# Optimization experiments

Hardware: AMD Instinct MI355X
Metric: run time of the kernel (lower is better)

Reference implementation:

```python
import jax, jax.numpy as jnp
import numpy as np

B = 256
WIN = 20          # input image side; 20 -> 12 -> 4 so num_routes = 32*4*4 = 512
ROUTES = 512
NCAPS = 10
DOUT = 16
DIN = 8
REC = 256 * WIN * WIN  # 102400


def _conv(x, w):
    return jax.lax.conv_general_dilated(x, w, (1, 1), 'VALID',
                                        dimension_numbers=('NCHW', 'OIHW', 'NCHW'))


def setup_inputs() -> dict:
    key = jax.random.key(0)
    ks = jax.random.split(key, 12)
    n = lambda k, shape, sc: (jax.random.normal(k, shape, jnp.float32) * sc)
    return {
        'data':    jax.random.normal(ks[0], (B, 1, WIN, WIN), jnp.float32),
        'conv1_w': n(ks[1], (256, 1, 9, 9), 0.1),
        'conv1_b': jnp.zeros((256,), jnp.float32),
        'prim_w':  n(ks[2], (8 * 32, 256, 9, 9), 0.007),  # 8 capsule convs fused: [8*32,256,9,9]
        'prim_b':  jnp.zeros((8 * 32,), jnp.float32),
        'W_digit': n(ks[3], (ROUTES, NCAPS, DOUT, DIN), 0.05),
        'dec_w1':  n(ks[4], (512, NCAPS * DOUT), 0.05),
        'dec_b1':  jnp.zeros((512,), jnp.float32),
        'dec_w2':  n(ks[5], (1024, 512), 0.04),
        'dec_b2':  jnp.zeros((1024,), jnp.float32),
        'dec_w3':  n(ks[6], (REC, 1024), 0.03),
        'dec_b3':  jnp.zeros((REC,), jnp.float32),
    }


def reference(data, conv1_w, conv1_b, prim_w, prim_b, W_digit,
              dec_w1, dec_b1, dec_w2, dec_b2, dec_w3, dec_b3):
    Bn = data.shape[0]
    # ConvLayer: 9x9 VALID conv + relu -> [B,256,12,12]
    h = jax.nn.relu(_conv(data, conv1_w) + conv1_b[None, :, None, None])
    # PrimaryCaps: 8 parallel convs (fused as one 256-out conv) -> [B,8,32,4,4]
    u = _conv(h, prim_w) + prim_b[None, :, None, None]
    H, W = u.shape[2], u.shape[3]
    u = u.reshape(Bn, 8, 32, H, W)
    # torch's u.view(B, 32*H*W, -1): raw row-major reshape of (8,32,H,W) -> (32*H*W, 8)
    u = u.reshape(Bn, 32 * H * W, 8)
    # vector squash over last (8-dim) axis
    sn = jnp.sum(u * u, axis=-1, keepdims=True)
    x = sn * u / ((1.0 + sn) * jnp.sqrt(sn))          # [B,R,8]
    # DigitCaps: u_hat[b,r,c,o] = W[r,c,o,i] x[b,r,i]
    u_hat = jnp.einsum('rcoi,bri->brco', W_digit, x)  # [B,R,10,16]
    b_ij = jnp.zeros((ROUTES, NCAPS), u_hat.dtype)    # shared over batch, as in original
    v = None
    for it in range(3):
        c = jax.nn.softmax(b_ij, axis=0)              # softmax over routes
        s = jnp.einsum('rc,brco->bco', c, u_hat)      # [B,10,16]
        # NOTE: original squash sums over a trailing dim of size 1 -> elementwise squash
        sq = s * s
        v = sq * s / ((1.0 + sq) * jnp.sqrt(sq))      # [B,10,16]
        if it < 2:
            a = jnp.einsum('brco,bco->brc', u_hat, v)
            b_ij = b_ij + jnp.mean(a, axis=0)
    # Decoder
    classes = jnp.sqrt(jnp.sum(v * v, axis=2))        # [B,10]
    classes = jax.nn.softmax(classes, axis=0)         # legacy F.softmax on 3D -> dim 0
    idx = jnp.argmax(classes, axis=1)                 # [B]
    masked = jax.nn.one_hot(idx, NCAPS, dtype=v.dtype)
    flat = (v * masked[:, :, None]).reshape(Bn, -1)   # [B,160]
    h1 = jax.nn.relu(flat @ dec_w1.T + dec_b1)
    h2 = jax.nn.relu(h1 @ dec_w2.T + dec_b2)
    rec = jax.nn.sigmoid(h2 @ dec_w3.T + dec_b3)
    return rec.reshape(-1, 256, WIN, WIN)
```

## Files before the change

kernel.cpp:

```cpp
#include <hip/hip_runtime.h>
#include <cmath>


constexpr int BATCH = 256;

enum { AM_PLAIN = 0, AM_CONV1 = 1 };
enum { EPI_NONE = 0, EPI_RELU = 1, EPI_SIG = 2, EPI_RELU_SPLIT = 3, EPI_RELU_H2B = 4 };

typedef short bf16x8 __attribute__((ext_vector_type(8)));
typedef unsigned short us8 __attribute__((ext_vector_type(8)));
typedef float f32x4 __attribute__((ext_vector_type(4)));

__device__ __forceinline__ unsigned short f2b(float v) {
  unsigned int u = __float_as_uint(v);
  u += 0x7FFFu + ((u >> 16) & 1u);
  return (unsigned short)(u >> 16);
}
__device__ __forceinline__ void split_bf(float v, unsigned short& h, unsigned short& l) {
  h = f2b(v);
  l = f2b(v - __uint_as_float(((unsigned int)h) << 16));
}

__device__ __forceinline__ void gload16(unsigned short* lds, const unsigned short* g) {
  __builtin_amdgcn_global_load_lds(
      (const __attribute__((address_space(1))) unsigned int*)(g),
      (__attribute__((address_space(3))) unsigned int*)(lds), 16, 0, 0);
}

template <int BM, int BN, int TM, int TN, int AMODE, int EPI>
__global__ __launch_bounds__(256, 2) void gemm_k(
    const float* __restrict__ A, const float* __restrict__ Bm,
    const float* __restrict__ bias, float* __restrict__ C,
    int M, int N, int K, int k_len,
    unsigned short* __restrict__ Chi, unsigned short* __restrict__ Clo) {
  static_assert(TM == 8 && TN == 8, "microtile fixed at 8x8");
  constexpr int BK = 8;
  constexpr int TX = BN / TN;

  const int tid = threadIdx.x;
  const int tx = tid % TX;
  const int ty = tid / TX;
  const int n0 = blockIdx.x * BN;
  const int m0 = blockIdx.y * BM;
  const int k_begin = blockIdx.z * k_len;
  const int k_end = k_begin + k_len;
  C += (size_t)blockIdx.z * (size_t)M * (size_t)N;

  __shared__ float As[BK][BM + 4];
  __shared__ float Bs[BK][BN + 4];

  float acc[TM][TN] = {};

  for (int kt = k_begin; kt < k_end; kt += BK) {
    __syncthreads();
    for (int base = tid * 4; base < BM * BK; base += 1024) {
      int ml = base / BK;
      int kl = base % BK;
#pragma unroll
      for (int j = 0; j < 4; j++) {
        int k = kt + kl + j;
        float v = 0.f;
        if (k < k_end) {
          if constexpr (AMODE == AM_PLAIN) {
            v = A[(size_t)(m0 + ml) * K + k];
          } else {
            int m = m0 + ml;
            int b = m / 144, p = m - b * 144;
            int py = p / 12, px = p - py * 12;
            int ky = k / 9, kx = k - ky * 9;
            v = A[b * 400 + (py + ky) * 20 + (px + kx)];
          }
        }
        As[kl + j][ml] = v;
      }
    }
    for (int base = tid * 4; base < BN * BK; base += 1024) {
      int nl = base / BK;
      int kl = base % BK;
#pragma unroll
      for (int j = 0; j < 4; j++) {
        int k = kt + kl + j;
        float v = 0.f;
        if (k < k_end) v = Bm[(size_t)(n0 + nl) * K + k];
        Bs[kl + j][nl] = v;
      }
    }
    __syncthreads();
#pragma unroll
    for (int kk = 0; kk < BK; kk++) {
      float af[TM], bf[TN];
      const float4* ap = reinterpret_cast<const float4*>(&As[kk][ty * TM]);
      reinterpret_cast<float4*>(af)[0] = ap[0];
      reinterpret_cast<float4*>(af)[1] = ap[1];
      const float4* bp = reinterpret_cast<const float4*>(&Bs[kk][tx * TN]);
      reinterpret_cast<float4*>(bf)[0] = bp[0];
      reinterpret_cast<float4*>(bf)[1] = bp[1];
#pragma unroll
      for (int i = 0; i < TM; i++)
#pragma unroll
        for (int j = 0; j < TN; j++) acc[i][j] += af[i] * bf[j];
    }
  }

#pragma unroll
  for (int i = 0; i < TM; i++) {
    int m = m0 + ty * TM + i;
#pragma unroll
    for (int j = 0; j < TN; j++) {
      int n = n0 + tx * TN + j;
      float v = acc[i][j];
      if constexpr (EPI == EPI_RELU) {
        v += bias[n];
        v = fmaxf(v, 0.f);
        C[(size_t)m * N + n] = v;
      } else if constexpr (EPI == EPI_SIG) {
        v += bias[n];
        v = 1.f / (1.f + expf(-v));
        C[(size_t)m * N + n] = v;
      } else if constexpr (EPI == EPI_RELU_SPLIT) {
        v += bias[n];
        v = fmaxf(v, 0.f);
        unsigned short hs, ls;
        split_bf(v, hs, ls);
        Chi[(size_t)m * N + n] = hs;
        Clo[(size_t)m * N + n] = ls;
      } else if constexpr (EPI == EPI_RELU_H2B) {
        v += bias[n];
        v = fmaxf(v, 0.f);
        Chi[(size_t)m * N + n] = f2b(v);
      } else {
        C[(size_t)m * N + n] = v;
      }
    }
  }
}

__global__ void transpose_w_k(const float* __restrict__ w,
                              unsigned short* __restrict__ hi,
                              unsigned short* __restrict__ lo) {
  __shared__ unsigned short shi[10368], slo[10368];
  const int n = blockIdx.x >> 1;
  const int h = blockIdx.x & 1;
  const int tid = threadIdx.x;
  const float* src = w + n * 20736 + h * 10368;
  for (int i = tid; i < 10368; i += 256) {
    float v = src[i];
    int cin_l = i / 81, kk = i - cin_l * 81;
    int idx = kk * 128 + ((cin_l + 2 * kk) & 127);
    unsigned short hb, lb;
    split_bf(v, hb, lb);
    shi[idx] = hb;
    slo[idx] = lb;
  }
  __syncthreads();
  unsigned short* dh = hi + n * 20736 + h * 128;
  unsigned short* dl = lo + n * 20736 + h * 128;
  for (int j = tid; j < 10368; j += 256) {
    int kk = j >> 7, cin_l = j & 127;
    int idx = (j & ~127) + ((cin_l + 2 * kk) & 127);
    dh[kk * 256 + cin_l] = shi[idx];
    dl[kk * 256 + cin_l] = slo[idx];
  }
}

__global__ __launch_bounds__(256, 2) void prim_mfma_k(
    const unsigned short* __restrict__ Ahi, const unsigned short* __restrict__ Alo,
    const unsigned short* __restrict__ Bhi, const unsigned short* __restrict__ Blo,
    float* __restrict__ part) {
  __shared__ unsigned short Ah[128 * 64], Al[128 * 64];
  __shared__ unsigned short Bh[128 * 64], Bl[128 * 64];

  const int tid = threadIdx.x;
  const int wave = tid >> 6, lane = tid & 63;
  const int wm = (wave >> 1) * 64, wn = (wave & 1) * 64;
  const int cl = lane & 15, rq = lane >> 4;
  const int n0 = blockIdx.x * 128;
  const int m0 = blockIdx.y * 128;
  const int z = blockIdx.z;
  const int k_begin = z * 1728, k_end = k_begin + 1728;

  int s_ldso[4];
  int s_arow[4];
  int s_cp8[4];
  size_t s_gb[4];
#pragma unroll
  for (int t = 0; t < 4; t++) {
    int g = (wave * 4 + t) * 64 + lane;
    int row = g >> 3, c = g & 7;
    int cp = c ^ (row & 7);
    s_ldso[t] = (wave * 4 + t) * 512;
    s_cp8[t] = cp * 8;
    int m = m0 + row;
    int b = m >> 4, q = m & 15;
    int y = q >> 2, xx = q & 3;
    s_arow[t] = b * 144 + y * 12 + xx;
    s_gb[t] = (size_t)(n0 + row) * 20736 + cp * 8;
  }

  f32x4 acc[4][4];
#pragma unroll
  for (int i = 0; i < 4; i++)
#pragma unroll
    for (int j = 0; j < 4; j++) acc[i][j] = f32x4{0.f, 0.f, 0.f, 0.f};

  for (int kt = k_begin; kt < k_end; kt += 64) {
    const int kk = kt >> 8;
    const int cin0 = kt & 255;
    const int dy = kk / 9, dx = kk - dy * 9;
    const int dyx = dy * 12 + dx;
    __syncthreads();
#pragma unroll
    for (int t = 0; t < 4; t++) {
      size_t ga = ((size_t)(s_arow[t] + dyx) << 8) + cin0 + s_cp8[t];
      size_t gb = s_gb[t] + kt;
      gload16(&Ah[s_ldso[t]], Ahi + ga);
      gload16(&Al[s_ldso[t]], Alo + ga);
      gload16(&Bh[s_ldso[t]], Bhi + gb);
      gload16(&Bl[s_ldso[t]], Blo + gb);
    }
    __syncthreads();

#pragma unroll
    for (int ko = 0; ko < 64; ko += 32) {
      const int cb = ko >> 3;
      bf16x8 a_hi[4], b_hi[4], t[4];
#pragma unroll
      for (int im = 0; im < 4; im++) {
        int r = wm + im * 16 + cl;
        a_hi[im] = *(const bf16x8*)&Ah[r * 64 + (((cb + rq) ^ (cl & 7)) << 3)];
      }
#pragma unroll
      for (int in = 0; in < 4; in++) {
        int r = wn + in * 16 + cl;
        b_hi[in] = *(const bf16x8*)&Bh[r * 64 + (((cb + rq) ^ (cl & 7)) << 3)];
      }
#pragma unroll
      for (int im = 0; im < 4; im++)
#pragma unroll
        for (int in = 0; in < 4; in++)
          acc[im][in] = __builtin_amdgcn_mfma_f32_16x16x32_bf16(a_hi[im], b_hi[in],
                                                                acc[im][in], 0, 0, 0);
#pragma unroll
      for (int in = 0; in < 4; in++) {
        int r = wn + in * 16 + cl;
        t[in] = *(const bf16x8*)&Bl[r * 64 + (((cb + rq) ^ (cl & 7)) << 3)];
      }
#pragma unroll
      for (int im = 0; im < 4; im++)
#pragma unroll
        for (int in = 0; in < 4; in++)
          acc[im][in] = __builtin_amdgcn_mfma_f32_16x16x32_bf16(a_hi[im], t[in],
                                                                acc[im][in], 0, 0, 0);
#pragma unroll
      for (int im = 0; im < 4; im++) {
        int r = wm + im * 16 + cl;
        t[im] = *(const bf16x8*)&Al[r * 64 + (((cb + rq) ^ (cl & 7)) << 3)];
      }
#pragma unroll
      for (int im = 0; im < 4; im++)
#pragma unroll
        for (int in = 0; in < 4; in++)
          acc[im][in] = __builtin_amdgcn_mfma_f32_16x16x32_bf16(t[im], b_hi[in],
                                                                acc[im][in], 0, 0, 0);
    }
  }

  float* Cp = part + (size_t)z * 1048576;
#pragma unroll
  for (int in = 0; in < 4; in++) {
    int n = n0 + wn + in * 16 + cl;
#pragma unroll
    for (int im = 0; im < 4; im++)
#pragma unroll
      for (int r = 0; r < 4; r++) {
        int m = m0 + wm + im * 16 + rq * 4 + r;
        Cp[(size_t)m * 256 + n] = acc[im][in][r];
      }
  }
}

__global__ __launch_bounds__(256, 2) void dec3_mfma_k(
    const unsigned short* __restrict__ Ab,
    const float* __restrict__ Bw,
    const float* __restrict__ bias,
    float* __restrict__ C) {
  constexpr int K = 1024, N = 102400;
  __shared__ unsigned short As[256 * 64];
  __shared__ unsigned short Bs[64 * 64];

  const int tid = threadIdx.x;
  const int wave = tid >> 6, lane = tid & 63;
  const int cl = lane & 15, rq = lane >> 4;
  const int n0 = blockIdx.x * 64;

  f32x4 acc[4][4];
#pragma unroll
  for (int i = 0; i < 4; i++)
#pragma unroll
    for (int j = 0; j < 4; j++) acc[i][j] = f32x4{0.f, 0.f, 0.f, 0.f};

  for (int kt = 0; kt < K; kt += 64) {
    __syncthreads();
#pragma unroll
    for (int j = 0; j < 8; j++) {
      int g = j * 256 + tid;
      int row = g >> 3, c = g & 7;
      int ld = row * 64 + ((c ^ (row & 7)) << 3);
      *(us8*)&As[ld] = *(const us8*)(Ab + (size_t)row * K + kt + c * 8);
    }
#pragma unroll
    for (int j = 0; j < 2; j++) {
      int g = j * 256 + tid;
      int row = g >> 3, c = g & 7;
      int ld = row * 64 + ((c ^ (row & 7)) << 3);
      const float* src = Bw + (size_t)(n0 + row) * K + kt + c * 8;
      float4 v0 = *(const float4*)src;
      float4 v1 = *(const float4*)(src + 4);
      us8 h;
      h[0] = f2b(v0.x); h[1] = f2b(v0.y); h[2] = f2b(v0.z); h[3] = f2b(v0.w);
      h[4] = f2b(v1.x); h[5] = f2b(v1.y); h[6] = f2b(v1.z); h[7] = f2b(v1.w);
      *(us8*)&Bs[ld] = h;
    }
    __syncthreads();
#pragma unroll
    for (int ko = 0; ko < 64; ko += 32) {
      const int cb = ko >> 3;
      bf16x8 af[4], bq[4];
#pragma unroll
      for (int im = 0; im < 4; im++) {
        int r = wave * 64 + im * 16 + cl;
        af[im] = *(const bf16x8*)&As[r * 64 + (((cb + rq) ^ (cl & 7)) << 3)];
      }
#pragma unroll
      for (int in = 0; in < 4; in++) {
        int r = in * 16 + cl;
        bq[in] = *(const bf16x8*)&Bs[r * 64 + (((cb + rq) ^ (cl & 7)) << 3)];
      }
#pragma unroll
      for (int im = 0; im < 4; im++)
#pragma unroll
        for (int in = 0; in < 4; in++)
          acc[im][in] = __builtin_amdgcn_mfma_f32_16x16x32_bf16(af[im], bq[in],
                                                                acc[im][in], 0, 0, 0);
    }
  }

#pragma unroll
  for (int in = 0; in < 4; in++) {
    int n = n0 + in * 16 + cl;
    float bn = bias[n];
#pragma unroll
    for (int im = 0; im < 4; im++)
#pragma unroll
      for (int r = 0; r < 4; r++) {
        int m = wave * 64 + im * 16 + rq * 4 + r;
        float v = acc[im][in][r] + bn;
        v = 1.f / (1.f + expf(-v));
        C[(size_t)m * N + n] = v;
      }
  }
}

__global__ void red_squash_k(const float* __restrict__ part,
                             const float* __restrict__ prim_b,
                             float* __restrict__ x) {
  const int chg = blockIdx.x;
  const int b = blockIdx.y;
  const int tid = threadIdx.x;
  const int ch_l = tid & 15;
  const int q = tid >> 4;
  const int ch = chg * 16 + ch_l;

  float val = prim_b[ch];
#pragma unroll
  for (int z = 0; z < 12; z++) val += part[z * 1048576 + (b * 16 + q) * 256 + ch];

  __shared__ float su[16][17];
  su[q][ch_l] = val;
  __syncthreads();

  const int vec = tid >> 3;
  const int i = tid & 7;
  const int ch_l2 = vec >> 1;
  const int t = vec & 1;
  float sn = 0.f;
#pragma unroll
  for (int ii = 0; ii < 8; ii++) {
    float e = su[8 * t + ii][ch_l2];
    sn += e * e;
  }
  float factor = sn / ((1.f + sn) * sqrtf(sn));
  float e = su[8 * t + i][ch_l2];
  int chh = chg * 16 + ch_l2;
  int d8 = chh >> 5, d32 = chh & 31;
  int r = d8 * 64 + d32 * 2 + t;
  x[b * 4096 + r * 8 + i] = e * factor;
}

__global__ void uhat_k(const float* __restrict__ W, const float* __restrict__ x,
                       float* __restrict__ uhat) {
  const int r = blockIdx.x;
  const int tid = threadIdx.x;
  __shared__ float Wl[8 * 160];
  __shared__ float xl[256 * 8];
  for (int t = tid; t < 1280; t += 256) {
    int co = t >> 3, i = t & 7;
    Wl[i * 160 + co] = W[r * 1280 + t];
  }
  for (int t = tid; t < 2048; t += 256) {
    int b = t >> 3, i = t & 7;
    xl[t] = x[b * 4096 + r * 8 + i];
  }
  __syncthreads();
  for (int item = tid; item < 256 * 160; item += 256) {
    int b = item / 160;
    int co = item - b * 160;
    float acc = 0.f;
#pragma unroll
    for (int i = 0; i < 8; i++) acc += Wl[i * 160 + co] * xl[b * 8 + i];
    uhat[b * 81920 + r * 160 + co] = acc;
  }
}

__global__ void zero_b_k(float* __restrict__ bij) {
  int id = blockIdx.x * 256 + threadIdx.x;
  if (id < 5120) bij[id] = 0.f;
}

__global__ void route_iter_k(const float* __restrict__ uhat,
                             const float* __restrict__ c_rc,
                             float* __restrict__ v_out,
                             float* __restrict__ a_buf,
                             int use_uniform, int do_update) {
  const int b = blockIdx.x;
  const int tid = threadIdx.x;
  __shared__ float c_l[5120];
  __shared__ float v_l[160];
  if (!use_uniform) {
    for (int t = tid; t < 5120; t += 256) c_l[t] = c_rc[t];
  }
  __syncthreads();
  if (tid < 160) {
    const float* up = uhat + b * 81920 + tid;
    const int cls = tid >> 4;
    float acc = 0.f;
    if (use_uniform) {
#pragma unroll 8
      for (int r = 0; r < 512; r++) acc += up[r * 160];
      acc *= (1.f / 512.f);
    } else {
#pragma unroll 8
      for (int r = 0; r < 512; r++) acc += c_l[r * 10 + cls] * up[r * 160];
    }
    float sq = acc * acc;
    float vv = sq * acc / ((1.f + sq) * sqrtf(sq));
    v_l[tid] = vv;
    v_out[b * 160 + tid] = vv;
  }
  __syncthreads();
  if (do_update) {
    for (int item = tid; item < 5120; item += 256) {
      int r = item / 10;
      int c = item - r * 10;
      const float* up2 = uhat + b * 81920 + r * 160 + c * 16;
      float a = 0.f;
#pragma unroll
      for (int o = 0; o < 16; o++) a += up2[o] * v_l[c * 16 + o];
      a_buf[b * 5120 + item] = a;
    }
  }
}

__global__ void bupd_k(const float* __restrict__ a_buf, float* __restrict__ bij) {
  int id = blockIdx.x * 256 + threadIdx.x;
  if (id >= 5120) return;
  float s = 0.f;
  for (int b = 0; b < BATCH; b++) s += a_buf[b * 5120 + id];
  bij[id] += s * (1.f / 256.f);
}

__global__ void softmax_b_k(const float* __restrict__ bij, float* __restrict__ c_rc) {
  const int tid = threadIdx.x;
  __shared__ float Ml[10], Sl[10];
  if (tid < 10) {
    float m = -1e30f;
    for (int r = 0; r < 512; r++) m = fmaxf(m, bij[r * 10 + tid]);
    float s = 0.f;
    for (int r = 0; r < 512; r++) s += expf(bij[r * 10 + tid] - m);
    Ml[tid] = m;
    Sl[tid] = s;
  }
  __syncthreads();
  if (tid < 512) {
    for (int c = 0; c < 10; c++)
      c_rc[tid * 10 + c] = expf(bij[tid * 10 + c] - Ml[c]) / Sl[c];
  }
}

__global__ void classes_k(const float* __restrict__ v, float* __restrict__ sel,
                          int* __restrict__ idxb) {
  const int b = threadIdx.x;
  float cl[10], ex[10];
  for (int c = 0; c < 10; c++) {
    float s = 0.f;
    for (int o = 0; o < 16; o++) {
      float e = v[b * 160 + c * 16 + o];
      s += e * e;
    }
    cl[c] = sqrtf(s);
  }
  __shared__ float red[256];
  __shared__ float Mc[10], Sc[10];
  for (int c = 0; c < 10; c++) {
    red[b] = cl[c];
    __syncthreads();
    for (int s = 128; s > 0; s >>= 1) {
      if (b < s) red[b] = fmaxf(red[b], red[b + s]);
      __syncthreads();
    }
    if (b == 0) Mc[c] = red[0];
    __syncthreads();
  }
  for (int c = 0; c < 10; c++) {
    ex[c] = expf(cl[c] - Mc[c]);
    red[b] = ex[c];
    __syncthreads();
    for (int s = 128; s > 0; s >>= 1) {
      if (b < s) red[b] += red[b + s];
      __syncthreads();
    }
    if (b == 0) Sc[c] = red[0];
    __syncthreads();
  }
  float best = ex[0] / Sc[0];
  int bi = 0;
  for (int c = 1; c < 10; c++) {
    float p = ex[c] / Sc[c];
    if (p > best) { best = p; bi = c; }
  }
  idxb[b] = bi;
  for (int o = 0; o < 16; o++) sel[b * 16 + o] = v[b * 160 + bi * 16 + o];
}

__global__ void h1_k(const float* __restrict__ sel, const int* __restrict__ idxb,
                     const float* __restrict__ w1, const float* __restrict__ b1,
                     float* __restrict__ h1) {
  const int b = blockIdx.x;
  const int j = threadIdx.x;
  __shared__ float ssel[16];
  __shared__ int six;
  if (j < 16) ssel[j] = sel[b * 16 + j];
  if (j == 0) six = idxb[b];
  __syncthreads();
  const float* wrow = w1 + j * 160 + six * 16;
  float acc = b1[j];
#pragma unroll
  for (int o = 0; o < 16; o++) acc += ssel[o] * wrow[o];
  h1[b * 512 + j] = fmaxf(acc, 0.f);
}

extern "C" void kernel_launch(void* const* d_in, const int* in_sizes, int n_in,
                              void* d_out, int out_size, void* d_ws, size_t ws_size,
                              hipStream_t stream) {
  const float* data    = (const float*)d_in[0];
  const float* conv1_w = (const float*)d_in[1];
  const float* conv1_b = (const float*)d_in[2];
  const float* prim_w  = (const float*)d_in[3];
  const float* prim_b  = (const float*)d_in[4];
  const float* W_digit = (const float*)d_in[5];
  const float* dec_w1  = (const float*)d_in[6];
  const float* dec_b1  = (const float*)d_in[7];
  const float* dec_w2  = (const float*)d_in[8];
  const float* dec_b2  = (const float*)d_in[9];
  const float* dec_w3  = (const float*)d_in[10];
  const float* dec_b3  = (const float*)d_in[11];
  float* out = (float*)d_out;

  float* ws = (float*)d_ws;
  float* uhat = ws;
  float* part = ws;
  unsigned short* h_hi  = (unsigned short*)(ws + 20971520);
  unsigned short* h_lo  = (unsigned short*)(ws + 25690112);
  unsigned short* wT_hi = (unsigned short*)(ws + 30408704);
  unsigned short* wT_lo = (unsigned short*)(ws + 33062912);
  float* x    = ws + 20971520;
  float* v    = ws + 22020096;
  float* bij  = ws + 22061056;
  float* crc  = ws + 22066176;
  float* abuf = ws + 22071296;
  float* sel  = ws + 23382016;
  int*   idxb = (int*)(ws + 23386112);
  float* h1   = ws + 23386368;
  unsigned short* h2b = (unsigned short*)(ws + 23517440);
  float* dummyC = ws + 23648512;

  transpose_w_k<<<512, 256, 0, stream>>>(prim_w, wT_hi, wT_lo);

  gemm_k<128, 128, 8, 8, AM_CONV1, EPI_RELU_SPLIT>
      <<<dim3(2, 288, 1), 256, 0, stream>>>(data, conv1_w, conv1_b, nullptr,
                                            36864, 256, 81, 81, h_hi, h_lo);

  prim_mfma_k<<<dim3(2, 32, 12), 256, 0, stream>>>(h_hi, h_lo, wT_hi, wT_lo, part);

  red_squash_k<<<dim3(16, 256), 256, 0, stream>>>(part, prim_b, x);

  uhat_k<<<512, 256, 0, stream>>>(W_digit, x, uhat);

  zero_b_k<<<20, 256, 0, stream>>>(bij);
  route_iter_k<<<256, 256, 0, stream>>>(uhat, crc, v, abuf, 1, 1);
  bupd_k<<<20, 256, 0, stream>>>(abuf, bij);
  softmax_b_k<<<1, 512, 0, stream>>>(bij, crc);
  route_iter_k<<<256, 256, 0, stream>>>(uhat, crc, v, abuf, 0, 1);
  bupd_k<<<20, 256, 0, stream>>>(abuf, bij);
  softmax_b_k<<<1, 512, 0, stream>>>(bij, crc);
  route_iter_k<<<256, 256, 0, stream>>>(uhat, crc, v, nullptr, 0, 0);

  classes_k<<<1, 256, 0, stream>>>(v, sel, idxb);

  h1_k<<<256, 512, 0, stream>>>(sel, idxb, dec_w1, dec_b1, h1);
  gemm_k<128, 128, 8, 8, AM_PLAIN, EPI_RELU_H2B>
      <<<dim3(8, 2, 1), 256, 0, stream>>>(h1, dec_w2, dec_b2, dummyC,
                                          256, 1024, 512, 512, h2b, nullptr);
  dec3_mfma_k<<<dim3(1600, 1, 1), 256, 0, stream>>>(h2b, dec_w3, dec_b3, out);
}
```

Baseline: 1.329 ms.

## Double-buffer primary-caps MFMA GEMM with larger tile; fuse routing softmax and classes kernels

The primary-caps bf16x3 GEMM now uses 512-thread blocks with a 256x128 tile and K-steps of 32. The next K-slice is loaded into a second LDS buffer while the current one is computed, and split-K drops from 12 to 8, so the reduction reads fewer partial buffers. The routing softmax over routes moves inside route_iter_k, and bij is initialised by the first update instead of a separate zero kernel. classes_k and h1_k are merged into one kernel, which removes several tiny launches. The catch is that LDS per block roughly doubles, which may limit occupancy, and the per-block softmax recompute is redundant across 256 blocks.

```diff
diff --git a/kernel.cpp b/kernel.cpp
--- a/kernel.cpp
+++ b/kernel.cpp
@@ -163,38 +163,43 @@
   }
 }
 
-__global__ __launch_bounds__(256, 2) void prim_mfma_k(
+__global__ __launch_bounds__(512, 2) void prim_mfma_k(
     const unsigned short* __restrict__ Ahi, const unsigned short* __restrict__ Alo,
     const unsigned short* __restrict__ Bhi, const unsigned short* __restrict__ Blo,
     float* __restrict__ part) {
-  __shared__ unsigned short Ah[128 * 64], Al[128 * 64];
-  __shared__ unsigned short Bh[128 * 64], Bl[128 * 64];
+  __shared__ __align__(16) unsigned short Ah[2 * 256 * 32], Al[2 * 256 * 32];
+  __shared__ __align__(16) unsigned short Bh[2 * 128 * 32], Bl[2 * 128 * 32];
 
   const int tid = threadIdx.x;
   const int wave = tid >> 6, lane = tid & 63;
   const int wm = (wave >> 1) * 64, wn = (wave & 1) * 64;
   const int cl = lane & 15, rq = lane >> 4;
   const int n0 = blockIdx.x * 128;
-  const int m0 = blockIdx.y * 128;
+  const int m0 = blockIdx.y * 256;
   const int z = blockIdx.z;
-  const int k_begin = z * 1728, k_end = k_begin + 1728;
-
-  int s_ldso[4];
-  int s_arow[4];
-  int s_cp8[4];
-  size_t s_gb[4];
-#pragma unroll
-  for (int t = 0; t < 4; t++) {
-    int g = (wave * 4 + t) * 64 + lane;
-    int row = g >> 3, c = g & 7;
-    int cp = c ^ (row & 7);
-    s_ldso[t] = (wave * 4 + t) * 512;
-    s_cp8[t] = cp * 8;
+  const int k_begin = z * 2592;
+  constexpr int NT = 81;
+
+  int a_ldso[2], a_row[2], a_cp8[2];
+#pragma unroll
+  for (int t = 0; t < 2; t++) {
+    int g = t * 512 + tid;
+    int row = g >> 2, c = g & 3;
+    int cp = c ^ (row & 3);
+    a_ldso[t] = g * 8;
+    a_cp8[t] = cp * 8;
     int m = m0 + row;
     int b = m >> 4, q = m & 15;
     int y = q >> 2, xx = q & 3;
-    s_arow[t] = b * 144 + y * 12 + xx;
-    s_gb[t] = (size_t)(n0 + row) * 20736 + cp * 8;
+    a_row[t] = b * 144 + y * 12 + xx;
+  }
+  int b_ldso;
+  size_t b_base;
+  {
+    int row = tid >> 2, c = tid & 3;
+    int cp = c ^ (row & 3);
+    b_ldso = tid * 8;
+    b_base = (size_t)(n0 + row) * 20736 + cp * 8;
   }
 
   f32x4 acc[4][4];
@@ -203,66 +208,73 @@
 #pragma unroll
     for (int j = 0; j < 4; j++) acc[i][j] = f32x4{0.f, 0.f, 0.f, 0.f};
 
-  for (int kt = k_begin; kt < k_end; kt += 64) {
+  auto STAGE = [&](int buf, int kt) {
     const int kk = kt >> 8;
     const int cin0 = kt & 255;
-    const int dy = kk / 9, dx = kk - dy * 9;
-    const int dyx = dy * 12 + dx;
-    __syncthreads();
-#pragma unroll
-    for (int t = 0; t < 4; t++) {
-      size_t ga = ((size_t)(s_arow[t] + dyx) << 8) + cin0 + s_cp8[t];
-      size_t gb = s_gb[t] + kt;
-      gload16(&Ah[s_ldso[t]], Ahi + ga);
-      gload16(&Al[s_ldso[t]], Alo + ga);
-      gload16(&Bh[s_ldso[t]], Bhi + gb);
-      gload16(&Bl[s_ldso[t]], Blo + gb);
-    }
-    __syncthreads();
-
-#pragma unroll
-    for (int ko = 0; ko < 64; ko += 32) {
-      const int cb = ko >> 3;
-      bf16x8 a_hi[4], b_hi[4], t[4];
-#pragma unroll
-      for (int im = 0; im < 4; im++) {
-        int r = wm + im * 16 + cl;
-        a_hi[im] = *(const bf16x8*)&Ah[r * 64 + (((cb + rq) ^ (cl & 7)) << 3)];
-      }
-#pragma unroll
-      for (int in = 0; in < 4; in++) {
-        int r = wn + in * 16 + cl;
-        b_hi[in] = *(const bf16x8*)&Bh[r * 64 + (((cb + rq) ^ (cl & 7)) << 3)];
-      }
-#pragma unroll
-      for (int im = 0; im < 4; im++)
-#pragma unroll
-        for (int in = 0; in < 4; in++)
-          acc[im][in] = __builtin_amdgcn_mfma_f32_16x16x32_bf16(a_hi[im], b_hi[in],
-                                                                acc[im][in], 0, 0, 0);
-#pragma unroll
-      for (int in = 0; in < 4; in++) {
-        int r = wn + in * 16 + cl;
-        t[in] = *(const bf16x8*)&Bl[r * 64 + (((cb + rq) ^ (cl & 7)) << 3)];
-      }
-#pragma unroll
-      for (int im = 0; im < 4; im++)
-#pragma unroll
-        for (int in = 0; in < 4; in++)
-          acc[im][in] = __builtin_amdgcn_mfma_f32_16x16x32_bf16(a_hi[im], t[in],
-                                                                acc[im][in], 0, 0, 0);
-#pragma unroll
-      for (int im = 0; im < 4; im++) {
-        int r = wm + im * 16 + cl;
-        t[im] = *(const bf16x8*)&Al[r * 64 + (((cb + rq) ^ (cl & 7)) << 3)];
-      }
-#pragma unroll
-      for (int im = 0; im < 4; im++)
-#pragma unroll
-        for (int in = 0; in < 4; in++)
-          acc[im][in] = __builtin_amdgcn_mfma_f32_16x16x32_bf16(t[im], b_hi[in],
-                                                                acc[im][in], 0, 0, 0);
-    }
+    const int dyx = (kk / 9) * 12 + (kk % 9);
+    const int ab = buf * 8192, bb = buf * 4096;
+#pragma unroll
+    for (int t = 0; t < 2; t++) {
+      size_t ga = ((size_t)(a_row[t] + dyx) << 8) + cin0 + a_cp8[t];
+      gload16(&Ah[ab + a_ldso[t]], Ahi + ga);
+      gload16(&Al[ab + a_ldso[t]], Alo + ga);
+    }
+    size_t gb = b_base + kt;
+    gload16(&Bh[bb + b_ldso], Bhi + gb);
+    gload16(&Bl[bb + b_ldso], Blo + gb);
+  };
+
+  auto COMPUTE = [&](int buf) {
+    const int ab = buf * 8192, bb = buf * 4096;
+    bf16x8 a_hi[4], b_hi[4], t[4];
+#pragma unroll
+    for (int im = 0; im < 4; im++) {
+      int r = wm + im * 16 + cl;
+      a_hi[im] = *(const bf16x8*)&Ah[ab + r * 32 + ((rq ^ (r & 3)) << 3)];
+    }
+#pragma unroll
+    for (int in = 0; in < 4; in++) {
+      int r = wn + in * 16 + cl;
+      b_hi[in] = *(const bf16x8*)&Bh[bb + r * 32 + ((rq ^ (r & 3)) << 3)];
+    }
+#pragma unroll
+    for (int im = 0; im < 4; im++)
+#pragma unroll
+      for (int in = 0; in < 4; in++)
+        acc[im][in] = __builtin_amdgcn_mfma_f32_16x16x32_bf16(a_hi[im], b_hi[in],
+                                                              acc[im][in], 0, 0, 0);
+#pragma unroll
+    for (int in = 0; in < 4; in++) {
+      int r = wn + in * 16 + cl;
+      t[in] = *(const bf16x8*)&Bl[bb + r * 32 + ((rq ^ (r & 3)) << 3)];
+    }
+#pragma unroll
+    for (int im = 0; im < 4; im++)
+#pragma unroll
+      for (int in = 0; in < 4; in++)
+        acc[im][in] = __builtin_amdgcn_mfma_f32_16x16x32_bf16(a_hi[im], t[in],
+                                                              acc[im][in], 0, 0, 0);
+#pragma unroll
+    for (int im = 0; im < 4; im++) {
+      int r = wm + im * 16 + cl;
+      t[im] = *(const bf16x8*)&Al[ab + r * 32 + ((rq ^ (r & 3)) << 3)];
+    }
+#pragma unroll
+    for (int im = 0; im < 4; im++)
+#pragma unroll
+      for (int in = 0; in < 4; in++)
+        acc[im][in] = __builtin_amdgcn_mfma_f32_16x16x32_bf16(t[im], b_hi[in],
+                                                              acc[im][in], 0, 0, 0);
+  };
+
+  STAGE(0, k_begin);
+  __syncthreads();
+  int cur = 0;
+  for (int ti = 0; ti < NT; ++ti) {
+    if (ti + 1 < NT) STAGE(cur ^ 1, k_begin + (ti + 1) * 32);
+    COMPUTE(cur);
+    __syncthreads();
+    cur ^= 1;
   }
 
   float* Cp = part + (size_t)z * 1048576;
@@ -285,8 +297,8 @@
     const float* __restrict__ bias,
     float* __restrict__ C) {
   constexpr int K = 1024, N = 102400;
-  __shared__ unsigned short As[256 * 64];
-  __shared__ unsigned short Bs[64 * 64];
+  __shared__ __align__(16) unsigned short As[256 * 64];
+  __shared__ __align__(16) unsigned short Bs[64 * 64];
 
   const int tid = threadIdx.x;
   const int wave = tid >> 6, lane = tid & 63;
@@ -373,7 +385,7 @@
 
   float val = prim_b[ch];
 #pragma unroll
-  for (int z = 0; z < 12; z++) val += part[z * 1048576 + (b * 16 + q) * 256 + ch];
+  for (int z = 0; z < 8; z++) val += part[z * 1048576 + (b * 16 + q) * 256 + ch];
 
   __shared__ float su[16][17];
   su[q][ch_l] = val;
@@ -422,13 +434,8 @@
   }
 }
 
-__global__ void zero_b_k(float* __restrict__ bij) {
-  int id = blockIdx.x * 256 + threadIdx.x;
-  if (id < 5120) bij[id] = 0.f;
-}
-
 __global__ void route_iter_k(const float* __restrict__ uhat,
-                             const float* __restrict__ c_rc,
+                             const float* __restrict__ bij,
                              float* __restrict__ v_out,
                              float* __restrict__ a_buf,
                              int use_uniform, int do_update) {
@@ -436,8 +443,40 @@
   const int tid = threadIdx.x;
   __shared__ float c_l[5120];
   __shared__ float v_l[160];
+  __shared__ float Ml[10], Sl[10], pm[10][16];
   if (!use_uniform) {
-    for (int t = tid; t < 5120; t += 256) c_l[t] = c_rc[t];
+    for (int t = tid; t < 5120; t += 256) c_l[t] = bij[t];
+    __syncthreads();
+    if (tid < 160) {
+      int c = tid >> 4, l = tid & 15;
+      float m = -1e30f;
+      for (int r = l; r < 512; r += 16) m = fmaxf(m, c_l[r * 10 + c]);
+      pm[c][l] = m;
+    }
+    __syncthreads();
+    if (tid < 10) {
+      float m = -1e30f;
+      for (int l = 0; l < 16; l++) m = fmaxf(m, pm[tid][l]);
+      Ml[tid] = m;
+    }
+    __syncthreads();
+    if (tid < 160) {
+      int c = tid >> 4, l = tid & 15;
+      float s = 0.f;
+      for (int r = l; r < 512; r += 16) s += expf(c_l[r * 10 + c] - Ml[c]);
+      pm[c][l] = s;
+    }
+    __syncthreads();
+    if (tid < 10) {
+      float s = 0.f;
+      for (int l = 0; l < 16; l++) s += pm[tid][l];
+      Sl[tid] = s;
+    }
+    __syncthreads();
+    for (int t = tid; t < 5120; t += 256) {
+      int c = t % 10;
+      c_l[t] = expf(c_l[t] - Ml[c]) / Sl[c];
+    }
   }
   __syncthreads();
   if (tid < 160) {
@@ -471,92 +510,63 @@
   }
 }
 
-__global__ void bupd_k(const float* __restrict__ a_buf, float* __restrict__ bij) {
+__global__ void bupd_k(const float* __restrict__ a_buf, float* __restrict__ bij,
+                       int first) {
   int id = blockIdx.x * 256 + threadIdx.x;
   if (id >= 5120) return;
   float s = 0.f;
   for (int b = 0; b < BATCH; b++) s += a_buf[b * 5120 + id];
-  bij[id] += s * (1.f / 256.f);
-}
-
-__global__ void softmax_b_k(const float* __restrict__ bij, float* __restrict__ c_rc) {
-  const int tid = threadIdx.x;
-  __shared__ float Ml[10], Sl[10];
+  s *= (1.f / 256.f);
+  bij[id] = first ? s : bij[id] + s;
+}
+
+__global__ void classes_h1_k(const float* __restrict__ v,
+                             const float* __restrict__ w1,
+                             const float* __restrict__ b1,
+                             float* __restrict__ h1) {
+  const int b = blockIdx.x;
+  const int tid = threadIdx.x;
+  __shared__ float ncl[2560];
+  __shared__ float Mc[10], Sc[10];
+  __shared__ float ssel[16];
+  __shared__ int sbi;
+  for (int item = tid; item < 2560; item += 512) {
+    int bb = item / 10, c = item - bb * 10;
+    float s = 0.f;
+#pragma unroll
+    for (int o = 0; o < 16; o++) {
+      float e = v[bb * 160 + c * 16 + o];
+      s += e * e;
+    }
+    ncl[item] = sqrtf(s);
+  }
+  __syncthreads();
   if (tid < 10) {
     float m = -1e30f;
-    for (int r = 0; r < 512; r++) m = fmaxf(m, bij[r * 10 + tid]);
+    for (int bb = 0; bb < 256; bb++) m = fmaxf(m, ncl[bb * 10 + tid]);
     float s = 0.f;
-    for (int r = 0; r < 512; r++) s += expf(bij[r * 10 + tid] - m);
-    Ml[tid] = m;
-    Sl[tid] = s;
-  }
-  __syncthreads();
-  if (tid < 512) {
-    for (int c = 0; c < 10; c++)
-      c_rc[tid * 10 + c] = expf(bij[tid * 10 + c] - Ml[c]) / Sl[c];
-  }
-}
-
-__global__ void classes_k(const float* __restrict__ v, float* __restrict__ sel,
-                          int* __restrict__ idxb) {
-  const int b = threadIdx.x;
-  float cl[10], ex[10];
-  for (int c = 0; c < 10; c++) {
-    float s = 0.f;
-    for (int o = 0; o < 16; o++) {
-      float e = v[b * 160 + c * 16 + o];
-      s += e * e;
-    }
-    cl[c] = sqrtf(s);
-  }
-  __shared__ float red[256];
-  __shared__ float Mc[10], Sc[10];
-  for (int c = 0; c < 10; c++) {
-    red[b] = cl[c];
-    __syncthreads();
-    for (int s = 128; s > 0; s >>= 1) {
-      if (b < s) red[b] = fmaxf(red[b], red[b + s]);
-      __syncthreads();
-    }
-    if (b == 0) Mc[c] = red[0];
-    __syncthreads();
-  }
-  for (int c = 0; c < 10; c++) {
-    ex[c] = expf(cl[c] - Mc[c]);
-    red[b] = ex[c];
-    __syncthreads();
-    for (int s = 128; s > 0; s >>= 1) {
-      if (b < s) red[b] += red[b + s];
-      __syncthreads();
-    }
-    if (b == 0) Sc[c] = red[0];
-    __syncthreads();
-  }
-  float best = ex[0] / Sc[0];
-  int bi = 0;
-  for (int c = 1; c < 10; c++) {
-    float p = ex[c] / Sc[c];
-    if (p > best) { best = p; bi = c; }
-  }
-  idxb[b] = bi;
-  for (int o = 0; o < 16; o++) sel[b * 16 + o] = v[b * 160 + bi * 16 + o];
-}
-
-__global__ void h1_k(const float* __restrict__ sel, const int* __restrict__ idxb,
-                     const float* __restrict__ w1, const float* __restrict__ b1,
-                     float* __restrict__ h1) {
-  const int b = blockIdx.x;
-  const int j = threadIdx.x;
-  __shared__ float ssel[16];
-  __shared__ int six;
-  if (j < 16) ssel[j] = sel[b * 16 + j];
-  if (j == 0) six = idxb[b];
-  __syncthreads();
-  const float* wrow = w1 + j * 160 + six * 16;
-  float acc = b1[j];
+    for (int bb = 0; bb < 256; bb++) s += expf(ncl[bb * 10 + tid] - m);
+    Mc[tid] = m;
+    Sc[tid] = s;
+  }
+  __syncthreads();
+  if (tid == 0) {
+    float best = -1e30f;
+    int bi = 0;
+    for (int c = 0; c < 10; c++) {
+      float p = expf(ncl[b * 10 + c] - Mc[c]) / Sc[c];
+      if (p > best) { best = p; bi = c; }
+    }
+    sbi = bi;
+  }
+  __syncthreads();
+  if (tid < 16) ssel[tid] = v[b * 160 + sbi * 16 + tid];
+  __syncthreads();
+  const float* wrow = w1 + tid * 160 + sbi * 16;
+  float acc = b1[tid];
 #pragma unroll
   for (int o = 0; o < 16; o++) acc += ssel[o] * wrow[o];
-  h1[b * 512 + j] = fmaxf(acc, 0.f);
+  h1[b * 512 + tid] = fmaxf(acc, 0.f);
 }
 
 extern "C" void kernel_launch(void* const* d_in, const int* in_sizes, int n_in,
@@ -586,10 +596,7 @@
   float* x    = ws + 20971520;
   float* v    = ws + 22020096;
   float* bij  = ws + 22061056;
-  float* crc  = ws + 22066176;
   float* abuf = ws + 22071296;
-  float* sel  = ws + 23382016;
-  int*   idxb = (int*)(ws + 23386112);
   float* h1   = ws + 23386368;
   unsigned short* h2b = (unsigned short*)(ws + 23517440);
   float* dummyC = ws + 23648512;
@@ -600,24 +607,20 @@
       <<<dim3(2, 288, 1), 256, 0, stream>>>(data, conv1_w, conv1_b, nullptr,
                                             36864, 256, 81, 81, h_hi, h_lo);
 
-  prim_mfma_k<<<dim3(2, 32, 12), 256, 0, stream>>>(h_hi, h_lo, wT_hi, wT_lo, part);
+  prim_mfma_k<<<dim3(2, 16, 8), 512, 0, stream>>>(h_hi, h_lo, wT_hi, wT_lo, part);
 
   red_squash_k<<<dim3(16, 256), 256, 0, stream>>>(part, prim_b, x);
 
   uhat_k<<<512, 256, 0, stream>>>(W_digit, x, uhat);
 
-  zero_b_k<<<20, 256, 0, stream>>>(bij);
-  route_iter_k<<<256, 256, 0, stream>>>(uhat, crc, v, abuf, 1, 1);
-  bupd_k<<<20, 256, 0, stream>>>(abuf, bij);
-  softmax_b_k<<<1, 512, 0, stream>>>(bij, crc);
-  route_iter_k<<<256, 256, 0, stream>>>(uhat, crc, v, abuf, 0, 1);
-  bupd_k<<<20, 256, 0, stream>>>(abuf, bij);
-  softmax_b_k<<<1, 512, 0, stream>>>(bij, crc);
-  route_iter_k<<<256, 256, 0, stream>>>(uhat, crc, v, nullptr, 0, 0);
-
-  classes_k<<<1, 256, 0, stream>>>(v, sel, idxb);
-
-  h1_k<<<256, 512, 0, stream>>>(sel, idxb, dec_w1, dec_b1, h1);
+  route_iter_k<<<256, 256, 0, stream>>>(uhat, bij, v, abuf, 1, 1);
+  bupd_k<<<20, 256, 0, stream>>>(abuf, bij, 1);
+  route_iter_k<<<256, 256, 0, stream>>>(uhat, bij, v, abuf, 0, 1);
+  bupd_k<<<20, 256, 0, stream>>>(abuf, bij, 0);
+  route_iter_k<<<256, 256, 0, stream>>>(uhat, bij, v, nullptr, 0, 0);
+
+  classes_h1_k<<<256, 512, 0, stream>>>(v, dec_w1, dec_b1, h1);
+
   gemm_k<128, 128, 8, 8, AM_PLAIN, EPI_RELU_H2B>
       <<<dim3(8, 2, 1), 256, 0, stream>>>(h1, dec_w2, dec_b2, dummyC,
                                           256, 1024, 512, 512, h2b, nullptr);
```

New measurement: 1.179 ms. -11.3%, faster.
